# Kernel tuning notes

Measured on AMD Instinct MI355X. Metric: run time of the kernel, lower is better.

## Reference

```python
import jax, jax.numpy as jnp
import numpy as np

D_MODEL = 1024
N_HEADS = 16
D_HEAD = D_MODEL // N_HEADS
D_FF = 4 * D_MODEL
SEQ = 2048
BATCH = 4
EPS = 1e-5


def setup_inputs() -> dict:
    key = jax.random.key(0)
    ks = jax.random.split(key, 12)
    s = 0.02
    return {
        "x": jax.random.normal(ks[0], (BATCH, SEQ, D_MODEL), dtype=jnp.float32),
        "ln1_g": jnp.ones((D_MODEL,), jnp.float32),
        "ln1_b": jnp.zeros((D_MODEL,), jnp.float32),
        "wq": jax.random.normal(ks[1], (N_HEADS, D_MODEL, D_HEAD), jnp.float32) * s,
        "bq": jnp.zeros((N_HEADS, D_HEAD), jnp.float32),
        "wk": jax.random.normal(ks[2], (N_HEADS, D_MODEL, D_HEAD), jnp.float32) * s,
        "bk": jnp.zeros((N_HEADS, D_HEAD), jnp.float32),
        "wv": jax.random.normal(ks[3], (N_HEADS, D_MODEL, D_HEAD), jnp.float32) * s,
        "bv": jnp.zeros((N_HEADS, D_HEAD), jnp.float32),
        "wp": jax.random.normal(ks[4], (D_MODEL, D_MODEL), jnp.float32) * s,
        "bp": jnp.zeros((D_MODEL,), jnp.float32),
        "ln2_g": jnp.ones((D_MODEL,), jnp.float32),
        "ln2_b": jnp.zeros((D_MODEL,), jnp.float32),
        "w1": jax.random.normal(ks[5], (D_MODEL, D_FF), jnp.float32) * s,
        "b1": jnp.zeros((D_FF,), jnp.float32),
        "w2": jax.random.normal(ks[6], (D_FF, D_MODEL), jnp.float32) * s,
        "b2": jnp.zeros((D_MODEL,), jnp.float32),
    }


def _layer_norm(x, g, b):
    mu = jnp.mean(x, axis=-1, keepdims=True)
    var = jnp.mean(jnp.square(x - mu), axis=-1, keepdims=True)
    return (x - mu) * jax.lax.rsqrt(var + EPS) * g + b


def _block(x, ln1_g, ln1_b, wq, bq, wk, bk, wv, bv, wp, bp,
           ln2_g, ln2_b, w1, b1, w2, b2):
    B, S, D = x.shape
    # --- pre-LN multi-head causal self-attention ---
    xn = _layer_norm(x, ln1_g, ln1_b)
    q = jnp.einsum('bsd,hde->bhse', xn, wq) + bq[None, :, None, :]
    k = jnp.einsum('bsd,hde->bhse', xn, wk) + bk[None, :, None, :]
    v = jnp.einsum('bsd,hde->bhse', xn, wv) + bv[None, :, None, :]
    scores = jnp.einsum('bhse,bhte->bhst', q, k) / np.sqrt(D_HEAD).astype(np.float32)
    causal = jnp.tril(jnp.ones((S, S), dtype=bool))
    scores = jnp.where(causal[None, None], scores, jnp.float32(-jnp.inf))
    attn = jax.nn.softmax(scores, axis=-1)
    o = jnp.einsum('bhst,bhte->bhse', attn, v)          # [B,H,S,Dh]
    o = o.transpose(0, 2, 1, 3).reshape(B, S, D)         # concat heads
    x = x + o @ wp + bp
    # --- pre-LN feedforward ---
    xn2 = _layer_norm(x, ln2_g, ln2_b)
    h = jax.nn.relu(xn2 @ w1 + b1)
    x = x + h @ w2 + b2
    return x


def reference(x, ln1_g, ln1_b, wq, bq, wk, bk, wv, bv, wp, bp,
              ln2_g, ln2_b, w1, b1, w2, b2):
    return _block(x, ln1_g, ln1_b, wq, bq, wk, bk, wv, bv, wp, bp,
                  ln2_g, ln2_b, w1, b1, w2, b2)
```

## Files before the change

kernel.cpp:

```cpp
#include <hip/hip_runtime.h>
#include <hip/hip_bf16.h>

#define D_MODEL 1024
#define N_HEADS 16
#define D_HEAD  64
#define D_FF    4096
#define SEQ     2048
#define BATCH   4
#define NROWS   (BATCH * SEQ)

typedef __attribute__((ext_vector_type(8))) short short8;
typedef __attribute__((ext_vector_type(4))) float f32x4;

#define EXP2(x) exp2f(x)
#define MFMA16(a, b, c) __builtin_amdgcn_mfma_f32_16x16x32_bf16(a, b, c, 0, 0, 0)

static __device__ __forceinline__ ushort f2bf(float x) {
  __hip_bfloat16 h = __float2bfloat16(x);
  return *reinterpret_cast<ushort*>(&h);
}

static __device__ __forceinline__ void gl_lds16(const ushort* g, ushort* l) {
  __builtin_amdgcn_global_load_lds(
      (const __attribute__((address_space(1))) void*)g,
      (__attribute__((address_space(3))) void*)l, 16, 0, 0);
}

__global__ __launch_bounds__(256) void transpose_pack_b(
    const float* __restrict__ in, ushort* __restrict__ out,
    int K, int N, size_t in_bs, size_t out_bs) {
  in  += (size_t)blockIdx.z * in_bs;
  out += (size_t)blockIdx.z * out_bs;
  __shared__ float tile[32][33];
  int n0 = blockIdx.x * 32, k0 = blockIdx.y * 32;
  int tx = threadIdx.x, ty = threadIdx.y;
#pragma unroll
  for (int i = 0; i < 32; i += 8)
    tile[ty + i][tx] = in[(size_t)(k0 + ty + i) * N + n0 + tx];
  __syncthreads();
#pragma unroll
  for (int i = 0; i < 32; i += 8)
    out[(size_t)(n0 + ty + i) * K + k0 + tx] = f2bf(tile[tx][ty + i]);
}

__global__ __launch_bounds__(256) void ln_kernel(
    const float* __restrict__ x, const float* __restrict__ g,
    const float* __restrict__ b, ushort* __restrict__ out) {
  int row = blockIdx.x, t = threadIdx.x;
  const float4 v = *(const float4*)(x + (size_t)row * D_MODEL + t * 4);
  float s  = v.x + v.y + v.z + v.w;
  float ss = v.x * v.x + v.y * v.y + v.z * v.z + v.w * v.w;
#pragma unroll
  for (int off = 1; off < 64; off <<= 1) {
    s  += __shfl_xor(s, off, 64);
    ss += __shfl_xor(ss, off, 64);
  }
  __shared__ float rs_[4], rss_[4];
  int w = t >> 6;
  if ((t & 63) == 0) { rs_[w] = s; rss_[w] = ss; }
  __syncthreads();
  s  = rs_[0] + rs_[1] + rs_[2] + rs_[3];
  ss = rss_[0] + rss_[1] + rss_[2] + rss_[3];
  float mu  = s * (1.0f / D_MODEL);
  float var = ss * (1.0f / D_MODEL) - mu * mu;
  float rstd = rsqrtf(var + 1e-5f);
  float4 gg = *(const float4*)(g + t * 4);
  float4 bb = *(const float4*)(b + t * 4);
  ushort4 r;
  r.x = f2bf((v.x - mu) * rstd * gg.x + bb.x);
  r.y = f2bf((v.y - mu) * rstd * gg.y + bb.y);
  r.z = f2bf((v.z - mu) * rstd * gg.z + bb.z);
  r.w = f2bf((v.w - mu) * rstd * gg.w + bb.w);
  *(ushort4*)(out + (size_t)row * D_MODEL + t * 4) = r;
}

template <int MODE>
__global__ __launch_bounds__(512, 2) void gemm256(
    const ushort* __restrict__ A, const ushort* __restrict__ BT,
    int M, int N, int K,
    const float* __restrict__ bias0, const float* __restrict__ bias1,
    const float* __restrict__ bias2,
    void* __restrict__ out0, void* __restrict__ out1, void* __restrict__ out2) {
  __shared__ __align__(16) ushort As[2][256 * 64];
  __shared__ __align__(16) ushort Bs[2][256 * 64];
  const int gx = N >> 8;
  const int nwg = gx * (M >> 8);
  const int cpx = nwg >> 3;
  const int tile = (blockIdx.x & 7) * cpx + (blockIdx.x >> 3);
  const int bn = tile % gx, bm = tile / gx;
  const int t = threadIdx.x, lane = t & 63, w = t >> 6;
  const int wr = w >> 2, wc = w & 3;
  const int l16 = lane & 15, l4 = lane >> 4;

  const ushort* Ab = A + (size_t)(bm * 256) * K;
  const ushort* Bb = BT + (size_t)(bn * 256) * K;

  int srow[4], scol[4];
#pragma unroll
  for (int i = 0; i < 4; ++i) {
    int c = i * 512 + t;
    srow[i] = c >> 3;
    scol[i] = 8 * ((c & 7) ^ ((c >> 3) & 7));
  }

  f32x4 acc[8][4] = {};
  int cur = 0;
  const int nk = K >> 6;

#pragma unroll
  for (int i = 0; i < 4; ++i) {
    gl_lds16(&Ab[(size_t)srow[i] * K + scol[i]], (ushort*)&As[0][(i * 512 + w * 64) * 8]);
    gl_lds16(&Bb[(size_t)srow[i] * K + scol[i]], (ushort*)&Bs[0][(i * 512 + w * 64) * 8]);
  }

  for (int kt = 0; kt < nk; ++kt) {
    if (kt + 1 < nk) {
      const int k0n = (kt + 1) << 6;
#pragma unroll
      for (int i = 0; i < 4; ++i) {
        gl_lds16(&Ab[(size_t)srow[i] * K + k0n + scol[i]], (ushort*)&As[cur ^ 1][(i * 512 + w * 64) * 8]);
        gl_lds16(&Bb[(size_t)srow[i] * K + k0n + scol[i]], (ushort*)&Bs[cur ^ 1][(i * 512 + w * 64) * 8]);
      }
      asm volatile("s_waitcnt vmcnt(8)" ::: "memory");
    } else {
      asm volatile("s_waitcnt vmcnt(0)" ::: "memory");
    }
    __builtin_amdgcn_s_barrier();

    const ushort* As_ = As[cur];
    const ushort* Bs_ = Bs[cur];
    short8 bfr[4][2];
#pragma unroll
    for (int n = 0; n < 4; ++n) {
      const int row = wc * 64 + n * 16 + l16;
      const int sw = (row & 7) * 8;
      bfr[n][0] = *(const short8*)&Bs_[row * 64 + ((l4 * 8) ^ sw)];
      bfr[n][1] = *(const short8*)&Bs_[row * 64 + ((l4 * 8 + 32) ^ sw)];
    }
#pragma unroll
    for (int m = 0; m < 8; ++m) {
      const int row = wr * 128 + m * 16 + l16;
      const int sw = (row & 7) * 8;
      short8 a0 = *(const short8*)&As_[row * 64 + ((l4 * 8) ^ sw)];
      short8 a1 = *(const short8*)&As_[row * 64 + ((l4 * 8 + 32) ^ sw)];
#pragma unroll
      for (int n = 0; n < 4; ++n) {
        acc[m][n] = MFMA16(a0, bfr[n][0], acc[m][n]);
        acc[m][n] = MFMA16(a1, bfr[n][1], acc[m][n]);
      }
    }
    asm volatile("" ::: "memory");
    __builtin_amdgcn_s_barrier();
    cur ^= 1;
  }

  const int row0 = bm * 256 + wr * 128, col0 = bn * 256 + wc * 64;
#pragma unroll
  for (int m = 0; m < 8; ++m) {
#pragma unroll
    for (int n = 0; n < 4; ++n) {
      const int col = col0 + n * 16 + l16;
      if (MODE == 0) {
        const int which = col >> 10;
        const int c = col & 1023;
        if (which < 2) {
          const float* bp_ = (which == 0) ? bias0 : bias1;
          ushort* op = (which == 0) ? (ushort*)out0 : (ushort*)out1;
          const float scale = (which == 0) ? 0.125f * 1.44269504f : 1.0f;
#pragma unroll
          for (int i = 0; i < 4; ++i) {
            const int row = row0 + m * 16 + l4 * 4 + i;
            op[(size_t)row * D_MODEL + c] = f2bf((acc[m][n][i] + bp_[c]) * scale);
          }
        } else {
          const int d = c & 63, hh2 = c >> 6;
          const float bv_ = bias2[c];
          ushort4 r4;
          r4.x = f2bf(acc[m][n][0] + bv_);
          r4.y = f2bf(acc[m][n][1] + bv_);
          r4.z = f2bf(acc[m][n][2] + bv_);
          r4.w = f2bf(acc[m][n][3] + bv_);
          const int row = row0 + m * 16 + l4 * 4;
          const int bb2 = row >> 11, s = row & 2047;
          *(ushort4*)((ushort*)out2 + ((size_t)(bb2 * 16 + hh2) * 64 + d) * SEQ + s) = r4;
        }
      } else {
#pragma unroll
        for (int i = 0; i < 4; ++i) {
          const int row = row0 + m * 16 + l4 * 4 + i;
          const float val = fmaxf(acc[m][n][i] + bias0[col], 0.0f);
          ((ushort*)out0)[(size_t)row * D_FF + col] = f2bf(val);
        }
      }
    }
  }
}

__global__ __launch_bounds__(256, 2) void gemm128d(
    const ushort* __restrict__ A, const ushort* __restrict__ BT,
    int M, int N, int K,
    const float* __restrict__ bias0, const float* __restrict__ resid,
    float* __restrict__ out0) {
  __shared__ __align__(16) ushort As[2][128 * 64];
  __shared__ __align__(16) ushort Bs[2][128 * 64];
  const int gx = N >> 7;
  const int nwg = gx * (M >> 7);
  const int cpx = nwg >> 3;
  const int tile = (blockIdx.x & 7) * cpx + (blockIdx.x >> 3);
  const int bn = tile % gx, bm = tile / gx;
  const int t = threadIdx.x, lane = t & 63, w = t >> 6;
  const int wr = w >> 1, wc = w & 1;
  const int l16 = lane & 15, l4 = lane >> 4;

  const ushort* Ab = A + (size_t)(bm * 128) * K;
  const ushort* Bb = BT + (size_t)(bn * 128) * K;

  int srow[4], scol[4];
#pragma unroll
  for (int i = 0; i < 4; ++i) {
    int c = i * 256 + t;
    srow[i] = c >> 3;
    scol[i] = 8 * ((c & 7) ^ ((c >> 3) & 7));
  }

  f32x4 acc[4][4] = {};
  int cur = 0;
  const int nk = K >> 6;

#pragma unroll
  for (int i = 0; i < 4; ++i) {
    gl_lds16(&Ab[(size_t)srow[i] * K + scol[i]], (ushort*)&As[0][(i * 256 + w * 64) * 8]);
    gl_lds16(&Bb[(size_t)srow[i] * K + scol[i]], (ushort*)&Bs[0][(i * 256 + w * 64) * 8]);
  }

  for (int kt = 0; kt < nk; ++kt) {
    if (kt + 1 < nk) {
      const int k0n = (kt + 1) << 6;
#pragma unroll
      for (int i = 0; i < 4; ++i) {
        gl_lds16(&Ab[(size_t)srow[i] * K + k0n + scol[i]], (ushort*)&As[cur ^ 1][(i * 256 + w * 64) * 8]);
        gl_lds16(&Bb[(size_t)srow[i] * K + k0n + scol[i]], (ushort*)&Bs[cur ^ 1][(i * 256 + w * 64) * 8]);
      }
      asm volatile("s_waitcnt vmcnt(8)" ::: "memory");
    } else {
      asm volatile("s_waitcnt vmcnt(0)" ::: "memory");
    }
    __builtin_amdgcn_s_barrier();

    const ushort* As_ = As[cur];
    const ushort* Bs_ = Bs[cur];
    short8 bfr[4][2];
#pragma unroll
    for (int n = 0; n < 4; ++n) {
      const int row = wc * 64 + n * 16 + l16;
      const int sw = (row & 7) * 8;
      bfr[n][0] = *(const short8*)&Bs_[row * 64 + ((l4 * 8) ^ sw)];
      bfr[n][1] = *(const short8*)&Bs_[row * 64 + ((l4 * 8 + 32) ^ sw)];
    }
#pragma unroll
    for (int m = 0; m < 4; ++m) {
      const int row = wr * 64 + m * 16 + l16;
      const int sw = (row & 7) * 8;
      short8 a0 = *(const short8*)&As_[row * 64 + ((l4 * 8) ^ sw)];
      short8 a1 = *(const short8*)&As_[row * 64 + ((l4 * 8 + 32) ^ sw)];
#pragma unroll
      for (int n = 0; n < 4; ++n) {
        acc[m][n] = MFMA16(a0, bfr[n][0], acc[m][n]);
        acc[m][n] = MFMA16(a1, bfr[n][1], acc[m][n]);
      }
    }
    asm volatile("" ::: "memory");
    __builtin_amdgcn_s_barrier();
    cur ^= 1;
  }

  const int row0 = bm * 128 + wr * 64, col0 = bn * 128 + wc * 64;
#pragma unroll
  for (int m = 0; m < 4; ++m) {
#pragma unroll
    for (int n = 0; n < 4; ++n) {
      const int col = col0 + n * 16 + l16;
#pragma unroll
      for (int i = 0; i < 4; ++i) {
        const int row = row0 + m * 16 + l4 * 4 + i;
        const size_t idx = (size_t)row * D_MODEL + col;
        out0[idx] = acc[m][n][i] + bias0[col] + resid[idx];
      }
    }
  }
}

__global__ __launch_bounds__(256) void attn8_kernel(
    const ushort* __restrict__ Q, const ushort* __restrict__ Km,
    const ushort* __restrict__ Vt, ushort* __restrict__ O) {
  const int b = blockIdx.x;
  const int bh = (b & 7) * 8 + ((b >> 3) & 7);
  const int p = b >> 6;
  const int bb = bh >> 4, hh = bh & 15;
  const int t = threadIdx.x, lane = t & 63, w = t >> 6;
  const int l16 = lane & 15, l4 = lane >> 4;
  const size_t base  = (size_t)bb * SEQ * D_MODEL + (size_t)hh * 64;
  const size_t vbase = (size_t)bh * 64 * SEQ;

  __shared__ __align__(16) ushort Ks[4][64 * 64];
  __shared__ __align__(16) ushort Vs[4][64 * 64];
  __shared__ __align__(16) ushort Pw[4][32 * 64];
  ushort* myP = &Pw[w][0];

#define STAGE(ktile, buf) do {                                                     \
    const int kv0_ = (ktile) * 64;                                                 \
    _Pragma("unroll")                                                              \
    for (int i_ = 0; i_ < 2; ++i_) {                                               \
      const int g_ = i_ * 256 + t;                                                 \
      const int row_ = g_ >> 3;                                                    \
      const int c8_ = ((g_ & 7) ^ (row_ & 7)) * 8;                                 \
      gl_lds16(&Km[base + (size_t)(kv0_ + row_) * D_MODEL + c8_],                  \
               (ushort*)&Ks[buf][(i_ * 256 + w * 64) * 8]);                        \
      gl_lds16(&Vt[vbase + (size_t)row_ * SEQ + kv0_ + c8_],                       \
               (ushort*)&Vs[buf][(i_ * 256 + w * 64) * 8]);                        \
    }                                                                              \
  } while (0)

#pragma unroll
  for (int pan = 0; pan < 2; ++pan) {
    const int qt = pan ? p : (15 - p);
    const int qb = qt * 128 + w * 32;
    const int nt = qt * 2 + 2;

    short8 qf[2][2];
#pragma unroll
    for (int qj = 0; qj < 2; ++qj)
#pragma unroll
      for (int dk = 0; dk < 2; ++dk)
        qf[qj][dk] = *(const short8*)&Q[base + (size_t)(qb + qj * 16 + l16) * D_MODEL + dk * 32 + l4 * 8];

    f32x4 oacc[4][2] = {};
    float l_i[2] = {0.0f, 0.0f};

    STAGE(0, 0);
    STAGE(1, 1);

    for (int jt = 0; jt < nt; jt += 2) {
      if (jt + 2 < nt) {
        STAGE(jt + 2, (jt + 2) & 3);
        STAGE(jt + 3, (jt + 3) & 3);
        asm volatile("s_waitcnt vmcnt(8)" ::: "memory");
      } else {
        asm volatile("s_waitcnt vmcnt(0)" ::: "memory");
      }
      __builtin_amdgcn_s_barrier();

#pragma unroll
      for (int half = 0; half < 2; ++half) {
        const int kt = jt + half;
        const int kv0 = kt * 64;
        const bool active = (kv0 <= qb + 31);
        if (active) {
          const ushort* Kc = Ks[kt & 3];
          const ushort* Vc = Vs[kt & 3];

          f32x4 sacc[2][4] = {};
#pragma unroll
          for (int n = 0; n < 4; ++n) {
            const int r = n * 16 + l16;
            const int rs = r * 8, rx = r & 7;
#pragma unroll
            for (int dk = 0; dk < 2; ++dk) {
              short8 ak = *(const short8*)&Kc[(rs + ((dk * 4 + l4) ^ rx)) * 8];
              sacc[0][n] = MFMA16(ak, qf[0][dk], sacc[0][n]);
              sacc[1][n] = MFMA16(ak, qf[1][dk], sacc[1][n]);
            }
          }

          const bool diag = (kv0 + 63 > qb);
#pragma unroll
          for (int qj = 0; qj < 2; ++qj) {
            const int qq = qb + qj * 16 + l16;
            const int ql = qj * 16 + l16;
            const int psw = (ql & 7) * 8;
            if (diag) {
#pragma unroll
              for (int n = 0; n < 4; ++n)
#pragma unroll
                for (int i = 0; i < 4; ++i) {
                  const int kv = kv0 + n * 16 + l4 * 4 + i;
                  if (kv > qq) sacc[qj][n][i] = -1e30f;
                }
            }
            float lsum = 0.0f;
#pragma unroll
            for (int n = 0; n < 4; ++n) {
              const float p0 = EXP2(sacc[qj][n][0]);
              const float p1 = EXP2(sacc[qj][n][1]);
              const float p2 = EXP2(sacc[qj][n][2]);
              const float p3 = EXP2(sacc[qj][n][3]);
              lsum += p0 + p1 + p2 + p3;
              ushort4 pk;
              pk.x = f2bf(p0); pk.y = f2bf(p1); pk.z = f2bf(p2); pk.w = f2bf(p3);
              *(ushort4*)&myP[ql * 64 + ((n * 16 + l4 * 4) ^ psw)] = pk;
            }
            l_i[qj] += lsum;
          }

#pragma unroll
          for (int kk = 0; kk < 2; ++kk) {
            short8 bp[2];
#pragma unroll
            for (int qj = 0; qj < 2; ++qj) {
              const int ql = qj * 16 + l16;
              bp[qj] = *(const short8*)&myP[ql * 64 + ((kk * 32 + l4 * 8) ^ ((ql & 7) * 8))];
            }
#pragma unroll
            for (int nd = 0; nd < 4; ++nd) {
              const int r = nd * 16 + l16;
              short8 av = *(const short8*)&Vc[(r * 8 + ((kk * 4 + l4) ^ (r & 7))) * 8];
              oacc[nd][0] = MFMA16(av, bp[0], oacc[nd][0]);
              oacc[nd][1] = MFMA16(av, bp[1], oacc[nd][1]);
            }
          }
        }
      }

      asm volatile("" ::: "memory");
      __builtin_amdgcn_s_barrier();
    }

#pragma unroll
    for (int qj = 0; qj < 2; ++qj) {
      l_i[qj] += __shfl_xor(l_i[qj], 16, 64);
      l_i[qj] += __shfl_xor(l_i[qj], 32, 64);
      const int qq = qb + qj * 16 + l16;
      const float inv = 1.0f / l_i[qj];
#pragma unroll
      for (int nd = 0; nd < 4; ++nd) {
        ushort4 r;
        r.x = f2bf(oacc[nd][qj][0] * inv);
        r.y = f2bf(oacc[nd][qj][1] * inv);
        r.z = f2bf(oacc[nd][qj][2] * inv);
        r.w = f2bf(oacc[nd][qj][3] * inv);
        *(ushort4*)&O[base + (size_t)qq * D_MODEL + nd * 16 + l4 * 4] = r;
      }
    }
  }
#undef STAGE
}

extern "C" void kernel_launch(void* const* d_in, const int* in_sizes, int n_in,
                              void* d_out, int out_size, void* d_ws, size_t ws_size,
                              hipStream_t stream) {
  const float* x    = (const float*)d_in[0];
  const float* ln1g = (const float*)d_in[1];
  const float* ln1b = (const float*)d_in[2];
  const float* wq   = (const float*)d_in[3];
  const float* bq   = (const float*)d_in[4];
  const float* wk   = (const float*)d_in[5];
  const float* bk   = (const float*)d_in[6];
  const float* wv   = (const float*)d_in[7];
  const float* bv   = (const float*)d_in[8];
  const float* wp   = (const float*)d_in[9];
  const float* bp   = (const float*)d_in[10];
  const float* ln2g = (const float*)d_in[11];
  const float* ln2b = (const float*)d_in[12];
  const float* w1   = (const float*)d_in[13];
  const float* b1   = (const float*)d_in[14];
  const float* w2   = (const float*)d_in[15];
  const float* b2   = (const float*)d_in[16];
  float* out = (float*)d_out;

  char* base = (char*)d_ws;
  size_t off = 0;
  auto alloc = [&](size_t bytes) -> void* {
    void* r = base + off;
    off += (bytes + 255) & ~(size_t)255;
    return r;
  };
  ushort* WqkvT = (ushort*)alloc((size_t)3 * D_MODEL * D_MODEL * 2);
  ushort* WpT   = (ushort*)alloc((size_t)D_MODEL * D_MODEL * 2);
  ushort* W1T   = (ushort*)alloc((size_t)D_FF * D_MODEL * 2);
  ushort* W2T   = (ushort*)alloc((size_t)D_MODEL * D_FF * 2);
  ushort* xn    = (ushort*)alloc((size_t)NROWS * D_MODEL * 2);
  ushort* q     = (ushort*)alloc((size_t)NROWS * D_MODEL * 2);
  ushort* k     = (ushort*)alloc((size_t)NROWS * D_MODEL * 2);
  ushort* vt    = (ushort*)alloc((size_t)NROWS * D_MODEL * 2);
  ushort* o     = (ushort*)alloc((size_t)NROWS * D_MODEL * 2);
  float*  x2    = (float*) alloc((size_t)NROWS * D_MODEL * 4);
  ushort* xn2   = (ushort*)alloc((size_t)NROWS * D_MODEL * 2);
  ushort* hbuf  = (ushort*)alloc((size_t)NROWS * D_FF * 2);

  dim3 tb(32, 8);
  transpose_pack_b<<<dim3(2, 32, 16), tb, 0, stream>>>(wq, WqkvT + (size_t)0 * D_MODEL * D_MODEL,
      D_MODEL, D_HEAD, (size_t)D_MODEL * D_HEAD, (size_t)D_HEAD * D_MODEL);
  transpose_pack_b<<<dim3(2, 32, 16), tb, 0, stream>>>(wk, WqkvT + (size_t)1 * D_MODEL * D_MODEL,
      D_MODEL, D_HEAD, (size_t)D_MODEL * D_HEAD, (size_t)D_HEAD * D_MODEL);
  transpose_pack_b<<<dim3(2, 32, 16), tb, 0, stream>>>(wv, WqkvT + (size_t)2 * D_MODEL * D_MODEL,
      D_MODEL, D_HEAD, (size_t)D_MODEL * D_HEAD, (size_t)D_HEAD * D_MODEL);
  transpose_pack_b<<<dim3(32, 32, 1), tb, 0, stream>>>(wp, WpT, D_MODEL, D_MODEL, 0, 0);
  transpose_pack_b<<<dim3(128, 32, 1), tb, 0, stream>>>(w1, W1T, D_MODEL, D_FF, 0, 0);
  transpose_pack_b<<<dim3(32, 128, 1), tb, 0, stream>>>(w2, W2T, D_FF, D_MODEL, 0, 0);

  ln_kernel<<<NROWS, 256, 0, stream>>>(x, ln1g, ln1b, xn);
  gemm256<0><<<dim3((NROWS / 256) * (3 * D_MODEL / 256)), 512, 0, stream>>>(
      xn, WqkvT, NROWS, 3 * D_MODEL, D_MODEL, bq, bk, bv, q, k, vt);
  attn8_kernel<<<512, 256, 0, stream>>>(q, k, vt, o);
  gemm128d<<<dim3((NROWS / 128) * (D_MODEL / 128)), 256, 0, stream>>>(
      o, WpT, NROWS, D_MODEL, D_MODEL, bp, x, x2);
  ln_kernel<<<NROWS, 256, 0, stream>>>(x2, ln2g, ln2b, xn2);
  gemm256<2><<<dim3((NROWS / 256) * (D_FF / 256)), 512, 0, stream>>>(
      xn2, W1T, NROWS, D_FF, D_MODEL, b1, nullptr, nullptr, hbuf, nullptr, nullptr);
  gemm128d<<<dim3((NROWS / 128) * (D_MODEL / 128)), 256, 0, stream>>>(
      hbuf, W2T, NROWS, D_MODEL, D_FF, b2, x2, out);
}
```

Measured before the change: 362.8 us.

## Use 32x32 MFMA in output GEMM and merge weight packing into one launch

The 128x128 residual-add GEMM now accumulates with 32x32x16 bf16 MFMA instructions on 2x2 tiles per wave instead of 16x16x32 on 4x4 tiles. This changes the LDS fragment load pattern and the epilogue row mapping. The aim is fewer LDS reads and MFMA issues per k-step. Separately, the six weight transpose/pack launches are merged into a single kernel driven by a block-index table, to cut launch overhead.

New measurement: 366.7 us. No clear change (+1.1%).

```diff
diff --git a/kernel.cpp b/kernel.cpp
--- a/kernel.cpp
+++ b/kernel.cpp
@@ -11,9 +11,11 @@
 
 typedef __attribute__((ext_vector_type(8))) short short8;
 typedef __attribute__((ext_vector_type(4))) float f32x4;
+typedef __attribute__((ext_vector_type(16))) float f32x16;
 
 #define EXP2(x) exp2f(x)
 #define MFMA16(a, b, c) __builtin_amdgcn_mfma_f32_16x16x32_bf16(a, b, c, 0, 0, 0)
+#define MFMA32(a, b, c) __builtin_amdgcn_mfma_f32_32x32x16_bf16(a, b, c, 0, 0, 0)
 
 static __device__ __forceinline__ ushort f2bf(float x) {
   __hip_bfloat16 h = __float2bfloat16(x);
@@ -26,14 +28,30 @@
       (__attribute__((address_space(3))) void*)l, 16, 0, 0);
 }
 
-__global__ __launch_bounds__(256) void transpose_pack_b(
-    const float* __restrict__ in, ushort* __restrict__ out,
-    int K, int N, size_t in_bs, size_t out_bs) {
-  in  += (size_t)blockIdx.z * in_bs;
-  out += (size_t)blockIdx.z * out_bs;
+struct PackArgs {
+  const float* in[6];
+  ushort* out[6];
+  int K[6], N[6], nx[6], per_batch[6];
+  long in_bs[6], out_bs[6];
+  int cum[7];
+};
+
+__global__ __launch_bounds__(256) void pack_all(PackArgs a) {
+  const int b = blockIdx.x;
+  int j = 0;
+#pragma unroll
+  for (int i = 0; i < 5; ++i) if (b >= a.cum[i + 1]) j = i + 1;
+  const int tidx = b - a.cum[j];
+  const int bz = tidx / a.per_batch[j];
+  const int rem = tidx % a.per_batch[j];
+  const int n0 = (rem % a.nx[j]) * 32;
+  const int k0 = (rem / a.nx[j]) * 32;
+  const float* in = a.in[j] + (long)bz * a.in_bs[j];
+  ushort* out = a.out[j] + (long)bz * a.out_bs[j];
+  const int K = a.K[j], N = a.N[j];
+
   __shared__ float tile[32][33];
-  int n0 = blockIdx.x * 32, k0 = blockIdx.y * 32;
-  int tx = threadIdx.x, ty = threadIdx.y;
+  const int tx = threadIdx.x, ty = threadIdx.y;
 #pragma unroll
   for (int i = 0; i < 32; i += 8)
     tile[ty + i][tx] = in[(size_t)(k0 + ty + i) * N + n0 + tx];
@@ -210,7 +228,7 @@
   const int bn = tile % gx, bm = tile / gx;
   const int t = threadIdx.x, lane = t & 63, w = t >> 6;
   const int wr = w >> 1, wc = w & 1;
-  const int l16 = lane & 15, l4 = lane >> 4;
+  const int l32 = lane & 31, lhi = lane >> 5;
 
   const ushort* Ab = A + (size_t)(bm * 128) * K;
   const ushort* Bb = BT + (size_t)(bn * 128) * K;
@@ -223,7 +241,7 @@
     scol[i] = 8 * ((c & 7) ^ ((c >> 3) & 7));
   }
 
-  f32x4 acc[4][4] = {};
+  f32x16 acc[2][2] = {};
   int cur = 0;
   const int nk = K >> 6;
 
@@ -233,6 +251,9 @@
     gl_lds16(&Bb[(size_t)srow[i] * K + scol[i]], (ushort*)&Bs[0][(i * 256 + w * 64) * 8]);
   }
 
+  const int ra0 = wr * 64 + l32,      ra1 = wr * 64 + 32 + l32;
+  const int rb0 = wc * 64 + l32,      rb1 = wc * 64 + 32 + l32;
+
   for (int kt = 0; kt < nk; ++kt) {
     if (kt + 1 < nk) {
       const int k0n = (kt + 1) << 6;
@@ -249,25 +270,17 @@
 
     const ushort* As_ = As[cur];
     const ushort* Bs_ = Bs[cur];
-    short8 bfr[4][2];
-#pragma unroll
-    for (int n = 0; n < 4; ++n) {
-      const int row = wc * 64 + n * 16 + l16;
-      const int sw = (row & 7) * 8;
-      bfr[n][0] = *(const short8*)&Bs_[row * 64 + ((l4 * 8) ^ sw)];
-      bfr[n][1] = *(const short8*)&Bs_[row * 64 + ((l4 * 8 + 32) ^ sw)];
-    }
-#pragma unroll
-    for (int m = 0; m < 4; ++m) {
-      const int row = wr * 64 + m * 16 + l16;
-      const int sw = (row & 7) * 8;
-      short8 a0 = *(const short8*)&As_[row * 64 + ((l4 * 8) ^ sw)];
-      short8 a1 = *(const short8*)&As_[row * 64 + ((l4 * 8 + 32) ^ sw)];
-#pragma unroll
-      for (int n = 0; n < 4; ++n) {
-        acc[m][n] = MFMA16(a0, bfr[n][0], acc[m][n]);
-        acc[m][n] = MFMA16(a1, bfr[n][1], acc[m][n]);
-      }
+#pragma unroll
+    for (int kk = 0; kk < 4; ++kk) {
+      const int g = kk * 2 + lhi;
+      short8 aF0 = *(const short8*)&As_[ra0 * 64 + ((g ^ (ra0 & 7)) * 8)];
+      short8 aF1 = *(const short8*)&As_[ra1 * 64 + ((g ^ (ra1 & 7)) * 8)];
+      short8 bF0 = *(const short8*)&Bs_[rb0 * 64 + ((g ^ (rb0 & 7)) * 8)];
+      short8 bF1 = *(const short8*)&Bs_[rb1 * 64 + ((g ^ (rb1 & 7)) * 8)];
+      acc[0][0] = MFMA32(aF0, bF0, acc[0][0]);
+      acc[0][1] = MFMA32(aF0, bF1, acc[0][1]);
+      acc[1][0] = MFMA32(aF1, bF0, acc[1][0]);
+      acc[1][1] = MFMA32(aF1, bF1, acc[1][1]);
     }
     asm volatile("" ::: "memory");
     __builtin_amdgcn_s_barrier();
@@ -276,15 +289,16 @@
 
   const int row0 = bm * 128 + wr * 64, col0 = bn * 128 + wc * 64;
 #pragma unroll
-  for (int m = 0; m < 4; ++m) {
-#pragma unroll
-    for (int n = 0; n < 4; ++n) {
-      const int col = col0 + n * 16 + l16;
-#pragma unroll
-      for (int i = 0; i < 4; ++i) {
-        const int row = row0 + m * 16 + l4 * 4 + i;
+  for (int mt = 0; mt < 2; ++mt) {
+#pragma unroll
+    for (int nt = 0; nt < 2; ++nt) {
+      const int col = col0 + nt * 32 + l32;
+      const float bc = bias0[col];
+#pragma unroll
+      for (int r = 0; r < 16; ++r) {
+        const int row = row0 + mt * 32 + (r & 3) + 8 * (r >> 2) + 4 * lhi;
         const size_t idx = (size_t)row * D_MODEL + col;
-        out0[idx] = acc[m][n][i] + bias0[col] + resid[idx];
+        out0[idx] = acc[mt][nt][r] + bc + resid[idx];
       }
     }
   }
@@ -487,16 +501,26 @@
   ushort* xn2   = (ushort*)alloc((size_t)NROWS * D_MODEL * 2);
   ushort* hbuf  = (ushort*)alloc((size_t)NROWS * D_FF * 2);
 
-  dim3 tb(32, 8);
-  transpose_pack_b<<<dim3(2, 32, 16), tb, 0, stream>>>(wq, WqkvT + (size_t)0 * D_MODEL * D_MODEL,
-      D_MODEL, D_HEAD, (size_t)D_MODEL * D_HEAD, (size_t)D_HEAD * D_MODEL);
-  transpose_pack_b<<<dim3(2, 32, 16), tb, 0, stream>>>(wk, WqkvT + (size_t)1 * D_MODEL * D_MODEL,
-      D_MODEL, D_HEAD, (size_t)D_MODEL * D_HEAD, (size_t)D_HEAD * D_MODEL);
-  transpose_pack_b<<<dim3(2, 32, 16), tb, 0, stream>>>(wv, WqkvT + (size_t)2 * D_MODEL * D_MODEL,
-      D_MODEL, D_HEAD, (size_t)D_MODEL * D_HEAD, (size_t)D_HEAD * D_MODEL);
-  transpose_pack_b<<<dim3(32, 32, 1), tb, 0, stream>>>(wp, WpT, D_MODEL, D_MODEL, 0, 0);
-  transpose_pack_b<<<dim3(128, 32, 1), tb, 0, stream>>>(w1, W1T, D_MODEL, D_FF, 0, 0);
-  transpose_pack_b<<<dim3(32, 128, 1), tb, 0, stream>>>(w2, W2T, D_FF, D_MODEL, 0, 0);
+  PackArgs pa;
+  pa.in[0] = wq; pa.out[0] = WqkvT + (size_t)0 * D_MODEL * D_MODEL;
+  pa.in[1] = wk; pa.out[1] = WqkvT + (size_t)1 * D_MODEL * D_MODEL;
+  pa.in[2] = wv; pa.out[2] = WqkvT + (size_t)2 * D_MODEL * D_MODEL;
+  pa.in[3] = wp; pa.out[3] = WpT;
+  pa.in[4] = w1; pa.out[4] = W1T;
+  pa.in[5] = w2; pa.out[5] = W2T;
+  for (int j = 0; j < 3; ++j) {
+    pa.K[j] = D_MODEL; pa.N[j] = D_HEAD; pa.nx[j] = 2; pa.per_batch[j] = 64;
+    pa.in_bs[j] = (long)D_MODEL * D_HEAD; pa.out_bs[j] = (long)D_HEAD * D_MODEL;
+  }
+  pa.K[3] = D_MODEL; pa.N[3] = D_MODEL; pa.nx[3] = 32; pa.per_batch[3] = 1024;
+  pa.in_bs[3] = 0; pa.out_bs[3] = 0;
+  pa.K[4] = D_MODEL; pa.N[4] = D_FF; pa.nx[4] = 128; pa.per_batch[4] = 4096;
+  pa.in_bs[4] = 0; pa.out_bs[4] = 0;
+  pa.K[5] = D_FF; pa.N[5] = D_MODEL; pa.nx[5] = 32; pa.per_batch[5] = 4096;
+  pa.in_bs[5] = 0; pa.out_bs[5] = 0;
+  pa.cum[0] = 0; pa.cum[1] = 1024; pa.cum[2] = 2048; pa.cum[3] = 3072;
+  pa.cum[4] = 4096; pa.cum[5] = 8192; pa.cum[6] = 12288;
+  pack_all<<<12288, dim3(32, 8), 0, stream>>>(pa);
 
   ln_kernel<<<NROWS, 256, 0, stream>>>(x, ln1g, ln1b, xn);
   gemm256<0><<<dim3((NROWS / 256) * (3 * D_MODEL / 256)), 512, 0, stream>>>(
```
